# Performance work log

Measured on AMD Instinct MI355X. Metric: run time of the kernel, lower is better.

## Reference

```python
import jax, jax.numpy as jnp
import numpy as np

_B, _F, _H, _W = 4, 256, 64, 64
_C, _S = 19, 256  # num_classes, memory-bank half size


def setup_inputs() -> dict:
    key = jax.random.key(0)
    k1, k2, k3, k4, k5 = jax.random.split(key, 5)
    memory_bank = jax.random.normal(k1, (_C, 2 * _S, _F), dtype=jnp.float32)
    pred_rep = jax.random.normal(k2, (_B, _F, _H, _W), dtype=jnp.float32)
    labels = jax.random.randint(k3, (_B, _H, _W), 0, _C)
    mask = jax.random.randint(k4, (_B, _H, _W), 0, 2).astype(bool)
    which_memory = jax.random.randint(k5, (_B, _H, _W), 0, 2)
    return {
        "memory_bank": memory_bank,
        "pred_rep": pred_rep,
        "labels": labels,
        "mask": mask,
        "which_memory": which_memory,
        "num_classes": _C,
    }


def reference(memory_bank, pred_rep, labels, mask, which_memory, num_classes, temp=0.5):
    eps = 1e-12
    C, twoS, F = memory_bank.shape
    S = twoS // 2
    # pixels-first layout: [P, F]
    feats = jnp.transpose(pred_rep, (0, 2, 3, 1)).reshape(-1, F)
    lab = labels.reshape(-1)
    msk = mask.reshape(-1)
    wm = which_memory.reshape(-1)
    mem = memory_bank.reshape(-1, F)  # [C*2S, F]
    fn = jnp.linalg.norm(feats, axis=1)  # [P]
    mn = jnp.linalg.norm(mem, axis=1)    # [C*2S]
    cos = (feats @ mem.T) / (fn[:, None] * mn[None, :])
    E = jnp.exp(cos / temp)              # [P, C*2S]
    Eb = E.reshape(-1, C, twoS)
    total = Eb.sum(axis=(1, 2))          # [P] sum over full bank
    block_sum = Eb.sum(axis=2)           # [P, C]
    loss = jnp.float32(0.0)
    class_count = jnp.float32(0.0)
    for i in range(num_classes):
        choice = msk & (lab == i)
        cnt = choice.sum()
        down = total - block_sum[:, i]   # negatives = all other classes
        block = Eb[:, i, :]              # [P, 2S] positives for class i
        contrib = jnp.float32(0.0)
        for net in range(2):
            sel = choice & (wm == 1 - net)
            pos = block[:, :S] if net == 0 else block[:, S:]
            term = -jnp.log(pos / (pos + down[:, None] + eps) + eps)
            contrib = contrib + jnp.where(sel[:, None], term, 0.0).sum()
        denom = jnp.maximum(cnt, 1).astype(jnp.float32) * S
        loss = loss + jnp.where(cnt > 0, contrib / denom, 0.0)
        class_count = class_count + (cnt > 0).astype(jnp.float32)
    return loss / jnp.maximum(class_count, 1.0)
```

## Files before the change

kernel.cpp:

```cpp
#include <hip/hip_runtime.h>
#include <hip/hip_bf16.h>
#include <math.h>

#define B_ 4
#define F_ 256
#define C_ 19
#define S_ 256
#define N_ 16384
#define M_ 9728
#define MT_ 38
#define PREP_PRED 256
#define PREP_BUCKET0 2688
#define GEMM_BLKS 512
#define P2_BLOCKS (C_ * 16)

typedef __bf16 bf16_t;
typedef bf16_t bf16x8 __attribute__((ext_vector_type(8)));
typedef float floatx4 __attribute__((ext_vector_type(4)));

#define AS1 __attribute__((address_space(1)))
#define AS3 __attribute__((address_space(3)))

__device__ inline size_t fragoff(int row, int f) {
    return ((size_t)((row >> 4) * 8 + (f >> 5))) * 512
         + (size_t)((((f >> 3) & 3) * 128) + ((row & 15) * 8) + (f & 7));
}

__global__ __launch_bounds__(256) void k_prep(const float* __restrict__ pred,
                                              const float* __restrict__ mem,
                                              __hip_bfloat16* __restrict__ A16f,
                                              __hip_bfloat16* __restrict__ B16,
                                              const int* __restrict__ labels,
                                              const int* __restrict__ mask,
                                              int* __restrict__ ccnt,
                                              int* __restrict__ pix) {
    int bid = blockIdx.x;
    int t = threadIdx.x;
    if (bid < PREP_PRED) {
        __shared__ float part[4][64];
        __shared__ float invf_s[64];
        int b = bid >> 6, hw0 = (bid & 63) * 64;
        int j = t & 63, q = t >> 6;
        int n0 = b * 4096 + hw0;

        const float* base = pred + ((size_t)b * F_ + q * 64) * 4096 + hw0 + j;
        float v[64];
        float s = 0.f;
        #pragma unroll
        for (int i = 0; i < 64; ++i) {
            float x = base[(size_t)i * 4096];
            v[i] = x;
            s += x * x;
        }
        part[q][j] = s;
        __syncthreads();
        if (t < 64) invf_s[t] = 1.0f / sqrtf(part[0][t] + part[1][t] + part[2][t] + part[3][t]);
        __syncthreads();
        float invf = invf_s[j];
        #pragma unroll
        for (int c = 0; c < 8; ++c) {
            int f = q * 64 + c * 8;
            __hip_bfloat16 tmp[8];
            #pragma unroll
            for (int u = 0; u < 8; ++u) tmp[u] = __float2bfloat16(v[c * 8 + u] * invf);
            *(float4*)&A16f[fragoff(n0 + j, f)] = *(float4*)tmp;
        }
    } else if (bid < PREP_BUCKET0) {
        int row  = (bid - PREP_PRED) * 4 + (t >> 6);
        int lane = t & 63;
        float4 a = ((const float4*)(mem + (size_t)row * F_))[lane];
        float s = a.x*a.x + a.y*a.y + a.z*a.z + a.w*a.w;
        #pragma unroll
        for (int off = 32; off; off >>= 1) s += __shfl_xor(s, off, 64);
        float invm = 1.0f / sqrtf(s);
        __hip_bfloat16 tmp[4];
        tmp[0] = __float2bfloat16(a.x * invm);
        tmp[1] = __float2bfloat16(a.y * invm);
        tmp[2] = __float2bfloat16(a.z * invm);
        tmp[3] = __float2bfloat16(a.w * invm);
        *(float2*)&B16[fragoff(row, lane * 4)] = *(float2*)tmp;
    } else {
        __shared__ int hist[C_], base_s[C_], cur[C_];
        int n0 = (bid - PREP_BUCKET0) * 256;
        if (t < C_) { hist[t] = 0; cur[t] = 0; }
        __syncthreads();
        int myc = labels[n0 + t];
        int mym = mask[n0 + t];
        if (mym) atomicAdd(&hist[myc], 1);
        __syncthreads();
        if (t < C_) base_s[t] = atomicAdd(&ccnt[t], hist[t]);
        __syncthreads();
        if (mym) {
            int o = atomicAdd(&cur[myc], 1);
            pix[myc * N_ + base_s[myc] + o] = n0 + t;
        }
    }
}

__global__ __launch_bounds__(512, 4) void k_pass1(const __hip_bfloat16* __restrict__ A16f,
                                                  const __hip_bfloat16* __restrict__ B16,
                                                  const int* __restrict__ ccnt,
                                                  const int* __restrict__ pix,
                                                  float* __restrict__ totpart) {
    __shared__ __hip_bfloat16 As[128 * 256];
    __shared__ float totals_s[2][4][128];
    __shared__ int pidx_s[128];
    int bid = blockIdx.x;
    int t = threadIdx.x;
    int w = t >> 6, lane = t & 63;
    int nh = w & 1, mq = w >> 1;

    int cnt_all = 0;
    #pragma unroll
    for (int cc = 0; cc < C_; ++cc) cnt_all += ccnt[cc];
    int nt_total = (cnt_all + 127) >> 7;
    if (nt_total == 0) return;
    int nchunk = GEMM_BLKS / nt_total;
    if (nchunk > MT_) nchunk = MT_;
    if (bid >= nt_total * nchunk) return;
    int panel = bid % nt_total;
    int chunk = bid / nt_total;
    int slot0 = panel * 128;

    if (t < 128) {
        int slot = slot0 + t;
        int run = 0, pixid = 0;
        #pragma unroll
        for (int cc = 0; cc < C_; ++cc) {
            int cn = ccnt[cc];
            if (slot >= run && slot < run + cn) pixid = pix[cc * N_ + slot - run];
            run += cn;
        }
        if (slot >= cnt_all) pixid = 0;
        pidx_s[t] = pixid;
    }
    __syncthreads();

    #pragma unroll
    for (int s = 0; s < 8; ++s) {
        int k = t + 512 * s;
        int row = ((k >> 9) << 4) | (k & 15);
        int f   = ((k >> 6) & 7) * 32 + ((k >> 4) & 3) * 8;
        float4 v = *(const float4*)&A16f[fragoff(pidx_s[row], f)];
        ((float4*)As)[k] = v;
    }
    __syncthreads();

    int colL = lane & 15, rgrp = (lane >> 4) * 4;
    int p = 0;
    for (int mt = chunk; mt < MT_; mt += nchunk, p ^= 1) {
        floatx4 acc[4][4];
        #pragma unroll
        for (int i = 0; i < 4; ++i)
            #pragma unroll
            for (int j2 = 0; j2 < 4; ++j2) acc[i][j2] = (floatx4){0.f, 0.f, 0.f, 0.f};

        const bf16x8* Bp = (const bf16x8*)B16 + ((size_t)(mt * 16 + mq * 4) * 8) * 64 + lane;

        #pragma unroll
        for (int kt = 0; kt < 8; ++kt) {
            bf16x8 af[4], bfr[4];
            #pragma unroll
            for (int ni = 0; ni < 4; ++ni)
                af[ni] = *(const bf16x8*)&As[((nh * 4 + ni) * 8 + kt) * 512 + lane * 8];
            #pragma unroll
            for (int mi = 0; mi < 4; ++mi)
                bfr[mi] = Bp[(size_t)(mi * 8 + kt) * 64];
            __builtin_amdgcn_s_setprio(1);
            #pragma unroll
            for (int ni = 0; ni < 4; ++ni)
                #pragma unroll
                for (int mi = 0; mi < 4; ++mi)
                    acc[ni][mi] = __builtin_amdgcn_mfma_f32_16x16x32_bf16(af[ni], bfr[mi], acc[ni][mi], 0, 0, 0);
            __builtin_amdgcn_s_setprio(0);
        }

        float racc[4][4];
        #pragma unroll
        for (int ni = 0; ni < 4; ++ni)
            #pragma unroll
            for (int r = 0; r < 4; ++r) racc[ni][r] = 0.f;
        #pragma unroll
        for (int ni = 0; ni < 4; ++ni)
            #pragma unroll
            for (int mi = 0; mi < 4; ++mi)
                #pragma unroll
                for (int r = 0; r < 4; ++r)
                    racc[ni][r] += __expf(2.0f * acc[ni][mi][r]);

        #pragma unroll
        for (int ni = 0; ni < 4; ++ni)
            #pragma unroll
            for (int r = 0; r < 4; ++r) {
                float s = racc[ni][r];
                s += __shfl_xor(s, 1, 64);
                s += __shfl_xor(s, 2, 64);
                s += __shfl_xor(s, 4, 64);
                s += __shfl_xor(s, 8, 64);
                if (colL == 0) totals_s[p][mq][nh * 64 + ni * 16 + rgrp + r] = s;
            }
        asm volatile("s_waitcnt lgkmcnt(0)\n\ts_barrier" ::: "memory");
        if (t < 128)
            totpart[(size_t)mt * N_ + slot0 + t] =
                totals_s[p][0][t] + totals_s[p][1][t] + totals_s[p][2][t] + totals_s[p][3][t];
    }
}

__global__ __launch_bounds__(512) void k_pass2(const __hip_bfloat16* __restrict__ A16f,
                                               const __hip_bfloat16* __restrict__ B16,
                                               const int* __restrict__ ccnt,
                                               const int* __restrict__ pix,
                                               const float* __restrict__ totpart,
                                               const int* __restrict__ wmem,
                                               float* __restrict__ class_sum,
                                               int* __restrict__ done,
                                               float* __restrict__ out) {
    __shared__ __hip_bfloat16 As[64 * 256];
    __shared__ int pidx_s[64];
    __shared__ float tot_s[64];
    __shared__ int wm_s[64];
    __shared__ float bsum_s[8][64];
    __shared__ float wsum_s[8][64];
    __shared__ float down_s[64];
    __shared__ float term_s[64];

    int c = blockIdx.x, tile = blockIdx.y;
    int cnt = ccnt[c];
    int t = threadIdx.x, ws = t >> 6, lane = t & 63;

    if (tile * 64 >= cnt) {
        if (t == 0) {
            __threadfence();
            int old = atomicAdd(done, 1);
            if (old == P2_BLOCKS - 1) {
                float loss = 0.f, kc = 0.f;
                for (int cc = 0; cc < C_; ++cc) {
                    int cn = ccnt[cc];
                    float sc = atomicAdd(&class_sum[cc], 0.f);
                    if (cn > 0) { loss += sc / ((float)cn * (float)S_); kc += 1.f; }
                }
                out[0] = loss / fmaxf(kc, 1.f);
            }
        }
        return;
    }

    int pre = 0;
    #pragma unroll
    for (int cc = 0; cc < C_; ++cc) if (cc < c) pre += ccnt[cc];
    int slot0 = pre + tile * 64;

    if (t < 64) {
        int i = tile * 64 + t;
        int p = pix[c * N_ + (i < cnt ? i : 0)];
        pidx_s[t] = p;
        wm_s[t]   = wmem[p];
    }
    __syncthreads();

    {
        int px = t >> 3, g = t & 7;
        float s = 0.f;
        for (int i = g; i < MT_; i += 8) s += totpart[(size_t)i * N_ + slot0 + px];
        s += __shfl_xor(s, 1, 64);
        s += __shfl_xor(s, 2, 64);
        s += __shfl_xor(s, 4, 64);
        if (g == 0) tot_s[px] = s;
    }

    #pragma unroll
    for (int s2 = 0; s2 < 4; ++s2) {
        int g = t + 512 * s2;
        int row = g >> 5, f = (g & 31) * 8;
        float4 v = *(const float4*)&A16f[fragoff(pidx_s[row], f)];
        *(float4*)&As[fragoff(row, f)] = v;
    }
    __syncthreads();

    floatx4 acc[4][4];
    #pragma unroll
    for (int i = 0; i < 4; ++i)
        #pragma unroll
        for (int j = 0; j < 4; ++j) acc[i][j] = (floatx4){0.f, 0.f, 0.f, 0.f};

    const bf16x8* Bp = (const bf16x8*)B16 + ((size_t)(c * 32 + ws * 4) * 8) * 64 + lane;
    #pragma unroll
    for (int kt = 0; kt < 8; ++kt) {
        bf16x8 af[4], bfr[4];
        #pragma unroll
        for (int ni = 0; ni < 4; ++ni)
            af[ni] = *(const bf16x8*)&As[(ni * 8 + kt) * 512 + lane * 8];
        #pragma unroll
        for (int mi = 0; mi < 4; ++mi) bfr[mi] = Bp[(size_t)(mi * 8 + kt) * 64];
        #pragma unroll
        for (int ni = 0; ni < 4; ++ni)
            #pragma unroll
            for (int mi = 0; mi < 4; ++mi)
                acc[ni][mi] = __builtin_amdgcn_mfma_f32_16x16x32_bf16(af[ni], bfr[mi], acc[ni][mi], 0, 0, 0);
    }

    int colL = lane & 15, rgrp = (lane >> 4) * 4;
    float Ev[4][4][4];
    #pragma unroll
    for (int ni = 0; ni < 4; ++ni)
        #pragma unroll
        for (int mi = 0; mi < 4; ++mi)
            #pragma unroll
            for (int r = 0; r < 4; ++r)
                Ev[ni][mi][r] = __expf(2.0f * acc[ni][mi][r]);

    #pragma unroll
    for (int ni = 0; ni < 4; ++ni)
        #pragma unroll
        for (int r = 0; r < 4; ++r) {
            float s = Ev[ni][0][r] + Ev[ni][1][r] + Ev[ni][2][r] + Ev[ni][3][r];
            s += __shfl_xor(s, 1, 64);
            s += __shfl_xor(s, 2, 64);
            s += __shfl_xor(s, 4, 64);
            s += __shfl_xor(s, 8, 64);
            if (colL == 0) bsum_s[ws][ni * 16 + rgrp + r] = s;
        }
    __syncthreads();
    if (t < 64) {
        float bs = 0.f;
        #pragma unroll
        for (int w2 = 0; w2 < 8; ++w2) bs += bsum_s[w2][t];
        down_s[t] = tot_s[t] - bs;
    }
    __syncthreads();

    #pragma unroll
    for (int ni = 0; ni < 4; ++ni)
        #pragma unroll
        for (int r = 0; r < 4; ++r) {
            int row = ni * 16 + rgrp + r;
            bool sel = (wm_s[row] == 1) ? (ws < 4) : (ws >= 4);
            float tt = 0.f;
            if (sel) {
                float dwn = down_s[row];
                #pragma unroll
                for (int mi = 0; mi < 4; ++mi) {
                    float pv = Ev[ni][mi][r];
                    tt += -logf(pv / (pv + dwn + 1e-12f) + 1e-12f);
                }
            }
            tt += __shfl_xor(tt, 1, 64);
            tt += __shfl_xor(tt, 2, 64);
            tt += __shfl_xor(tt, 4, 64);
            tt += __shfl_xor(tt, 8, 64);
            if (colL == 0) wsum_s[ws][row] = tt;
        }
    __syncthreads();
    if (t < 64) {
        int i = tile * 64 + t;
        float s = 0.f;
        if (i < cnt) {
            #pragma unroll
            for (int w2 = 0; w2 < 8; ++w2) s += wsum_s[w2][t];
        }
        term_s[t] = s;
    }
    __syncthreads();
    if (t < 64) {
        float s = term_s[t];
        #pragma unroll
        for (int off = 1; off < 64; off <<= 1) s += __shfl_xor(s, off, 64);
        if (t == 0) {
            atomicAdd(&class_sum[c], s);
            __threadfence();
            int old = atomicAdd(done, 1);
            if (old == P2_BLOCKS - 1) {
                float loss = 0.f, kc = 0.f;
                for (int cc = 0; cc < C_; ++cc) {
                    int cn = ccnt[cc];
                    float sc = atomicAdd(&class_sum[cc], 0.f);
                    if (cn > 0) { loss += sc / ((float)cn * (float)S_); kc += 1.f; }
                }
                out[0] = loss / fmaxf(kc, 1.f);
            }
        }
    }
}

extern "C" void kernel_launch(void* const* d_in, const int* in_sizes, int n_in,
                              void* d_out, int out_size, void* d_ws, size_t ws_size,
                              hipStream_t stream) {
    const float* mem    = (const float*)d_in[0];
    const float* pred   = (const float*)d_in[1];
    const int*   labels = (const int*)  d_in[2];
    const int*   mask   = (const int*)  d_in[3];
    const int*   wmem   = (const int*)  d_in[4];
    float* out = (float*)d_out;

    float* ws = (float*)d_ws;
    float* totpart   = ws;
    int*   ctrl      = (int*)(ws + 622592);
    int*   ccnt      = ctrl;
    float* class_sum = (float*)(ctrl + 19);
    int*   done      = ctrl + 38;
    int*   pix       = (int*)(ws + 622640);
    __hip_bfloat16* A16f = (__hip_bfloat16*)(ws + 933936);
    __hip_bfloat16* B16  = (__hip_bfloat16*)(ws + 3031088);

    hipMemsetAsync(ctrl, 0, 40 * sizeof(int), stream);

    k_prep<<<PREP_BUCKET0 + 64, 256, 0, stream>>>(pred, mem, A16f, B16,
                                                  labels, mask, ccnt, pix);

    k_pass1<<<GEMM_BLKS, 512, 0, stream>>>(A16f, B16, ccnt, pix, totpart);

    dim3 g2(C_, 16);
    k_pass2<<<g2, 512, 0, stream>>>(A16f, B16, ccnt, pix, totpart, wmem,
                                    class_sum, done, out);
}
```

Before: 177.2 us.

## Add compaction kernel gathering selected pixels into class-padded contiguous fragment buffer

```diff
diff --git a/kernel.cpp b/kernel.cpp
--- a/kernel.cpp
+++ b/kernel.cpp
@@ -9,6 +9,7 @@
 #define N_ 16384
 #define M_ 9728
 #define MT_ 38
+#define NP_ 18816
 #define PREP_PRED 256
 #define PREP_BUCKET0 2688
 #define GEMM_BLKS 512
@@ -97,52 +98,65 @@
     }
 }
 
-__global__ __launch_bounds__(512, 4) void k_pass1(const __hip_bfloat16* __restrict__ A16f,
+__global__ __launch_bounds__(256) void k_compact(const __hip_bfloat16* __restrict__ A16f,
+                                                 const int* __restrict__ ccnt,
+                                                 const int* __restrict__ pix,
+                                                 __hip_bfloat16* __restrict__ A16c) {
+    __shared__ int pidx_s[64];
+    int bid = blockIdx.x, t = threadIdx.x;
+    int slot0 = bid * 64;
+    int slot = slot0 + (t & 63);
+    int run = 0, pixid = 0;
+    #pragma unroll
+    for (int cc = 0; cc < C_; ++cc) {
+        int cn = ccnt[cc];
+        if (slot >= run && slot < run + cn) pixid = pix[cc * N_ + slot - run];
+        run += (cn + 127) & ~127;
+    }
+    if (slot0 >= run) return;
+    if (t < 64) pidx_s[t] = pixid;
+    __syncthreads();
+    #pragma unroll
+    for (int s = 0; s < 8; ++s) {
+        int k = t + 256 * s;
+        int row = ((k >> 9) << 4) | (k & 15);
+        int f   = ((k >> 6) & 7) * 32 + ((k >> 4) & 3) * 8;
+        float4 v = *(const float4*)&A16f[fragoff(pidx_s[row], f)];
+        *(float4*)&A16c[((size_t)slot0 << 8) + (size_t)k * 8] = v;
+    }
+}
+
+__global__ __launch_bounds__(512, 4) void k_pass1(const __hip_bfloat16* __restrict__ A16c,
                                                   const __hip_bfloat16* __restrict__ B16,
                                                   const int* __restrict__ ccnt,
-                                                  const int* __restrict__ pix,
                                                   float* __restrict__ totpart) {
     __shared__ __hip_bfloat16 As[128 * 256];
     __shared__ float totals_s[2][4][128];
-    __shared__ int pidx_s[128];
     int bid = blockIdx.x;
     int t = threadIdx.x;
     int w = t >> 6, lane = t & 63;
     int nh = w & 1, mq = w >> 1;
 
-    int cnt_all = 0;
-    #pragma unroll
-    for (int cc = 0; cc < C_; ++cc) cnt_all += ccnt[cc];
-    int nt_total = (cnt_all + 127) >> 7;
+    int padded_total = 0;
+    #pragma unroll
+    for (int cc = 0; cc < C_; ++cc) padded_total += (ccnt[cc] + 127) & ~127;
+    int nt_total = padded_total >> 7;
     if (nt_total == 0) return;
     int nchunk = GEMM_BLKS / nt_total;
     if (nchunk > MT_) nchunk = MT_;
+    if (nchunk < 1) nchunk = 1;
     if (bid >= nt_total * nchunk) return;
     int panel = bid % nt_total;
     int chunk = bid / nt_total;
-    int slot0 = panel * 128;
-
-    if (t < 128) {
-        int slot = slot0 + t;
-        int run = 0, pixid = 0;
-        #pragma unroll
-        for (int cc = 0; cc < C_; ++cc) {
-            int cn = ccnt[cc];
-            if (slot >= run && slot < run + cn) pixid = pix[cc * N_ + slot - run];
-            run += cn;
-        }
-        if (slot >= cnt_all) pixid = 0;
-        pidx_s[t] = pixid;
-    }
-    __syncthreads();
-
-    #pragma unroll
-    for (int s = 0; s < 8; ++s) {
-        int k = t + 512 * s;
-        int row = ((k >> 9) << 4) | (k & 15);
-        int f   = ((k >> 6) & 7) * 32 + ((k >> 4) & 3) * 8;
-        float4 v = *(const float4*)&A16f[fragoff(pidx_s[row], f)];
-        ((float4*)As)[k] = v;
+    int slot0 = panel << 7;
+
+    {
+        const __hip_bfloat16* src = A16c + ((size_t)slot0 << 8) + w * 4096 + lane * 8;
+        __hip_bfloat16* dst = &As[w * 4096];
+        #pragma unroll
+        for (int i = 0; i < 8; ++i)
+            __builtin_amdgcn_global_load_lds((const AS1 unsigned int*)(src + i * 512),
+                                             (AS3 unsigned int*)(dst + i * 512), 16, 0, 0);
     }
     __syncthreads();
 
@@ -201,12 +215,12 @@
             }
         asm volatile("s_waitcnt lgkmcnt(0)\n\ts_barrier" ::: "memory");
         if (t < 128)
-            totpart[(size_t)mt * N_ + slot0 + t] =
+            totpart[(size_t)mt * NP_ + slot0 + t] =
                 totals_s[p][0][t] + totals_s[p][1][t] + totals_s[p][2][t] + totals_s[p][3][t];
     }
 }
 
-__global__ __launch_bounds__(512) void k_pass2(const __hip_bfloat16* __restrict__ A16f,
+__global__ __launch_bounds__(512) void k_pass2(const __hip_bfloat16* __restrict__ A16c,
                                                const __hip_bfloat16* __restrict__ B16,
                                                const int* __restrict__ ccnt,
                                                const int* __restrict__ pix,
@@ -216,7 +230,6 @@
                                                int* __restrict__ done,
                                                float* __restrict__ out) {
     __shared__ __hip_bfloat16 As[64 * 256];
-    __shared__ int pidx_s[64];
     __shared__ float tot_s[64];
     __shared__ int wm_s[64];
     __shared__ float bsum_s[8][64];
@@ -247,33 +260,32 @@
 
     int pre = 0;
     #pragma unroll
-    for (int cc = 0; cc < C_; ++cc) if (cc < c) pre += ccnt[cc];
+    for (int cc = 0; cc < C_; ++cc) if (cc < c) pre += (ccnt[cc] + 127) & ~127;
     int slot0 = pre + tile * 64;
+
+    {
+        const __hip_bfloat16* src = A16c + ((size_t)slot0 << 8) + t * 8;
+        __hip_bfloat16* dst = &As[t * 8];
+        #pragma unroll
+        for (int i = 0; i < 4; ++i)
+            __builtin_amdgcn_global_load_lds((const AS1 unsigned int*)(src + i * 4096),
+                                             (AS3 unsigned int*)(dst + i * 4096), 16, 0, 0);
+    }
 
     if (t < 64) {
         int i = tile * 64 + t;
         int p = pix[c * N_ + (i < cnt ? i : 0)];
-        pidx_s[t] = p;
-        wm_s[t]   = wmem[p];
-    }
-    __syncthreads();
+        wm_s[t] = wmem[p];
+    }
 
     {
         int px = t >> 3, g = t & 7;
         float s = 0.f;
-        for (int i = g; i < MT_; i += 8) s += totpart[(size_t)i * N_ + slot0 + px];
+        for (int i = g; i < MT_; i += 8) s += totpart[(size_t)i * NP_ + slot0 + px];
         s += __shfl_xor(s, 1, 64);
         s += __shfl_xor(s, 2, 64);
         s += __shfl_xor(s, 4, 64);
         if (g == 0) tot_s[px] = s;
-    }
-
-    #pragma unroll
-    for (int s2 = 0; s2 < 4; ++s2) {
-        int g = t + 512 * s2;
-        int row = g >> 5, f = (g & 31) * 8;
-        float4 v = *(const float4*)&A16f[fragoff(pidx_s[row], f)];
-        *(float4*)&As[fragoff(row, f)] = v;
     }
     __syncthreads();
 
@@ -394,22 +406,25 @@
 
     float* ws = (float*)d_ws;
     float* totpart   = ws;
-    int*   ctrl      = (int*)(ws + 622592);
+    int*   ctrl      = (int*)(ws + 715008);
     int*   ccnt      = ctrl;
     float* class_sum = (float*)(ctrl + 19);
     int*   done      = ctrl + 38;
-    int*   pix       = (int*)(ws + 622640);
-    __hip_bfloat16* A16f = (__hip_bfloat16*)(ws + 933936);
-    __hip_bfloat16* B16  = (__hip_bfloat16*)(ws + 3031088);
+    int*   pix       = (int*)(ws + 715048);
+    __hip_bfloat16* A16f = (__hip_bfloat16*)(ws + 1026344);
+    __hip_bfloat16* A16c = (__hip_bfloat16*)(ws + 3123496);
+    __hip_bfloat16* B16  = (__hip_bfloat16*)(ws + 5531944);
 
     hipMemsetAsync(ctrl, 0, 40 * sizeof(int), stream);
 
     k_prep<<<PREP_BUCKET0 + 64, 256, 0, stream>>>(pred, mem, A16f, B16,
                                                   labels, mask, ccnt, pix);
 
-    k_pass1<<<GEMM_BLKS, 512, 0, stream>>>(A16f, B16, ccnt, pix, totpart);
+    k_compact<<<NP_ / 64, 256, 0, stream>>>(A16f, ccnt, pix, A16c);
+
+    k_pass1<<<GEMM_BLKS, 512, 0, stream>>>(A16c, B16, ccnt, totpart);
 
     dim3 g2(C_, 16);
-    k_pass2<<<g2, 512, 0, stream>>>(A16f, B16, ccnt, pix, totpart, wmem,
+    k_pass2<<<g2, 512, 0, stream>>>(A16c, B16, ccnt, pix, totpart, wmem,
                                     class_sum, done, out);
 }
```

Result: no change. 176.3 us (-0.5%).
